# Performance work log

Measured on AMD Instinct MI355X. Metric: run time of the kernel, lower is better.

Reference implementation:

```python
import jax, jax.numpy as jnp
import numpy as np


def setup_inputs() -> dict:
    key = jax.random.key(0)
    ks = jax.random.split(key, 8)
    N, T, U = 8, 512, 64
    E, D, J, V = 512, 512, 512, 500
    s = 0.02
    return {
        "encoder_out": jax.random.normal(ks[0], (N, T, E), jnp.float32),
        "decoder_out": jax.random.normal(ks[1], (N, U, D), jnp.float32),
        "W_enc": jax.random.normal(ks[2], (J, E), jnp.float32) * s,
        "b_enc": jnp.zeros((J,), jnp.float32),
        "W_dec": jax.random.normal(ks[3], (J, D), jnp.float32) * s,
        "b_dec": jnp.zeros((J,), jnp.float32),
        "W_out": jax.random.normal(ks[4], (V, J), jnp.float32) * s,
        "b_out": jnp.zeros((V,), jnp.float32),
    }


def reference(encoder_out, decoder_out, W_enc, b_enc, W_dec, b_dec, W_out, b_out):
    # Project encoder [N,T,E]->[N,T,J] and decoder [N,U,D]->[N,U,J]
    enc = jnp.einsum("nte,je->ntj", encoder_out, W_enc) + b_enc
    dec = jnp.einsum("nud,jd->nuj", decoder_out, W_dec) + b_dec
    # Broadcast add over (T,U), tanh, then vocab projection -> [N,T,U,V]
    activations = jnp.tanh(enc[:, :, None, :] + dec[:, None, :, :])
    logits = jnp.einsum("ntuj,vj->ntuv", activations, W_out) + b_out
    return logits
```

## Files before the change

### kernel.cpp

```cpp
#include <hip/hip_runtime.h>
#include <hip/hip_bf16.h>


typedef __attribute__((ext_vector_type(4))) float f32x4;
typedef __attribute__((ext_vector_type(16))) float f32x16;
typedef __attribute__((ext_vector_type(4))) short s16x4;
typedef __attribute__((ext_vector_type(8))) short s16x8;
typedef __attribute__((ext_vector_type(4))) unsigned short u16x4;

static __device__ __forceinline__ unsigned short f2bf(float x) {
    union { float f; unsigned u; } v; v.f = x;
    return (unsigned short)((v.u + 0x7FFFu + ((v.u >> 16) & 1u)) >> 16);
}

static __device__ __forceinline__ float bf2f(unsigned short u) {
    union { unsigned u; float f; } v; v.u = ((unsigned)u) << 16;
    return v.f;
}

static __device__ __forceinline__ float fast_tanh(float x) {
    float e = __expf(2.0f * x);
    float r = __builtin_amdgcn_rcpf(e + 1.0f);
    return __builtin_fmaf(-2.0f, r, 1.0f);
}

static __device__ __forceinline__ unsigned swz64(int r, int c) {
    return (unsigned)(r * 64 + ((c ^ ((r >> 1) & 3)) << 4));
}

static __device__ void proj_body(
    const float* __restrict__ A, const float* __restrict__ W,
    const float* __restrict__ b, unsigned short* __restrict__ C,
    int mt, int jt, unsigned short* As, unsigned short* Bs)
{
    const int tid = threadIdx.x;
    const int lane = tid & 63, wid = tid >> 6;
    const int wm = wid >> 1, wn = wid & 1;

    f32x4 acc[4][4];
    const f32x4 zero = {0.f, 0.f, 0.f, 0.f};
    #pragma unroll
    for (int i = 0; i < 4; ++i)
        #pragma unroll
        for (int j = 0; j < 4; ++j) acc[i][j] = zero;

    const int c8 = (tid & 7) * 8;
    const int rbase = tid >> 3;

    for (int kt = 0; kt < 8; ++kt) {
        __syncthreads();
        #pragma unroll
        for (int p = 0; p < 4; ++p) {
            int r = p * 32 + rbase;
            int byte = (r * 128 + c8 * 2) ^ ((r & 7) << 4);
            {
                const float* s = A + (size_t)(mt * 128 + r) * 512 + kt * 64 + c8;
                f32x4 v0 = *(const f32x4*)s, v1 = *(const f32x4*)(s + 4);
                s16x8 pk;
                pk[0] = (short)f2bf(v0[0]); pk[1] = (short)f2bf(v0[1]);
                pk[2] = (short)f2bf(v0[2]); pk[3] = (short)f2bf(v0[3]);
                pk[4] = (short)f2bf(v1[0]); pk[5] = (short)f2bf(v1[1]);
                pk[6] = (short)f2bf(v1[2]); pk[7] = (short)f2bf(v1[3]);
                *(s16x8*)((char*)As + byte) = pk;
            }
            {
                const float* s = W + (size_t)(jt * 128 + r) * 512 + kt * 64 + c8;
                f32x4 v0 = *(const f32x4*)s, v1 = *(const f32x4*)(s + 4);
                s16x8 pk;
                pk[0] = (short)f2bf(v0[0]); pk[1] = (short)f2bf(v0[1]);
                pk[2] = (short)f2bf(v0[2]); pk[3] = (short)f2bf(v0[3]);
                pk[4] = (short)f2bf(v1[0]); pk[5] = (short)f2bf(v1[1]);
                pk[6] = (short)f2bf(v1[2]); pk[7] = (short)f2bf(v1[3]);
                *(s16x8*)((char*)Bs + byte) = pk;
            }
        }
        __syncthreads();
        #pragma unroll
        for (int kk = 0; kk < 2; ++kk) {
            s16x8 af[4], bfr[4];
            #pragma unroll
            for (int mi = 0; mi < 4; ++mi) {
                int row = wm * 64 + mi * 16 + (lane & 15);
                int byte = (row * 128 + kk * 64 + ((lane >> 4) * 16)) ^ ((row & 7) << 4);
                af[mi] = *(const s16x8*)((const char*)As + byte);
            }
            #pragma unroll
            for (int ni = 0; ni < 4; ++ni) {
                int row = wn * 64 + ni * 16 + (lane & 15);
                int byte = (row * 128 + kk * 64 + ((lane >> 4) * 16)) ^ ((row & 7) << 4);
                bfr[ni] = *(const s16x8*)((const char*)Bs + byte);
            }
            #pragma unroll
            for (int mi = 0; mi < 4; ++mi)
                #pragma unroll
                for (int ni = 0; ni < 4; ++ni)
                    acc[mi][ni] = __builtin_amdgcn_mfma_f32_16x16x32_bf16(
                        af[mi], bfr[ni], acc[mi][ni], 0, 0, 0);
        }
    }

    #pragma unroll
    for (int ni = 0; ni < 4; ++ni) {
        int col = jt * 128 + wn * 64 + ni * 16 + (lane & 15);
        float bias = b[col];
        #pragma unroll
        for (int mi = 0; mi < 4; ++mi) {
            int row0 = mt * 128 + wm * 64 + mi * 16 + ((lane >> 4) << 2);
            #pragma unroll
            for (int j = 0; j < 4; ++j)
                C[(size_t)(row0 + j) * 512 + col] = f2bf(acc[mi][ni][j] + bias);
        }
    }
}

__global__ __launch_bounds__(256) void prep(
    const float* __restrict__ Wout, unsigned short* __restrict__ img,
    const float* __restrict__ encoder_out, const float* __restrict__ W_enc,
    const float* __restrict__ b_enc, unsigned short* __restrict__ enc_p,
    const float* __restrict__ decoder_out, const float* __restrict__ W_dec,
    const float* __restrict__ b_dec, unsigned short* __restrict__ dec_p,
    const float* __restrict__ b_out, float* __restrict__ bpad)
{
    __shared__ unsigned short As[128 * 64];
    __shared__ unsigned short Bs[128 * 64];
    const int b = blockIdx.x;
    if (b < 128) {
        int tid = b * 256 + threadIdx.x;
        int lane = tid & 63;
        int khalf = (tid >> 6) & 1;
        int tile = (tid >> 7) & 15;
        int kt = tid >> 11;
        int v = tile * 32 + (lane & 31);
        int k = kt * 32 + khalf * 16 + (lane >> 5) * 8;
        s16x8 pk = {0, 0, 0, 0, 0, 0, 0, 0};
        if (v < 500) {
            const float* s = Wout + (size_t)v * 512 + k;
            f32x4 a = *(const f32x4*)s, c = *(const f32x4*)(s + 4);
            pk[0] = (short)f2bf(a[0]); pk[1] = (short)f2bf(a[1]);
            pk[2] = (short)f2bf(a[2]); pk[3] = (short)f2bf(a[3]);
            pk[4] = (short)f2bf(c[0]); pk[5] = (short)f2bf(c[1]);
            pk[6] = (short)f2bf(c[2]); pk[7] = (short)f2bf(c[3]);
        }
        *(s16x8*)(img + (size_t)tid * 8) = pk;
    } else if (b < 256) {
        int q = b - 128;
        proj_body(encoder_out, W_enc, b_enc, enc_p, q & 31, q >> 5, As, Bs);
    } else if (b < 272) {
        int q = b - 256;
        proj_body(decoder_out, W_dec, b_dec, dec_p, q & 3, q >> 2, As, Bs);
    } else {
        int i = threadIdx.x;
        bpad[i] = (i < 500) ? b_out[i] : 0.f;
        bpad[i + 256] = (i + 256 < 500) ? b_out[i + 256] : 0.f;
    }
}

__global__ __launch_bounds__(512, 4) void joiner_main(
    const unsigned short* __restrict__ enc, const unsigned short* __restrict__ dec,
    const unsigned short* __restrict__ Wimg, const float* __restrict__ bout,
    float* __restrict__ out)
{
    __shared__ __align__(16) char raw[66048];
    unsigned short* As0 = (unsigned short*)raw;
    unsigned short* As1 = (unsigned short*)(raw + 4096);
    float* ep = (float*)raw;

    const int bid = blockIdx.x;
    const int tid = threadIdx.x, lane = tid & 63, wn = tid >> 6;
    const int n = bid >> 9, t = bid & 511;

    f32x16 acc[2][2];
    #pragma unroll
    for (int i = 0; i < 2; ++i)
        #pragma unroll
        for (int j = 0; j < 2; ++j)
            #pragma unroll
            for (int e = 0; e < 16; ++e) acc[i][j][e] = 0.f;

    const int r = tid >> 3;
    const int q = tid & 7;
    const unsigned short* erow = enc + ((size_t)n * 512 + t) * 512 + q * 4;
    const unsigned short* drow = dec + ((size_t)n * 64 + r) * 512 + q * 4;
    const unsigned abyte = swz64(r, q >> 1) + (q & 1) * 8;
    const char* wbase = (const char*)Wimg + (size_t)wn * 4096 + (size_t)lane * 16;
    const int lr = lane & 31, kg = lane >> 5;

    {
        u16x4 e = *(const u16x4*)erow;
        u16x4 d = *(const u16x4*)drow;
        s16x4 p;
        p[0] = (short)f2bf(fast_tanh(bf2f(e[0]) + bf2f(d[0])));
        p[1] = (short)f2bf(fast_tanh(bf2f(e[1]) + bf2f(d[1])));
        p[2] = (short)f2bf(fast_tanh(bf2f(e[2]) + bf2f(d[2])));
        p[3] = (short)f2bf(fast_tanh(bf2f(e[3]) + bf2f(d[3])));
        *(s16x4*)((char*)As0 + abyte) = p;
    }
    __syncthreads();

    #pragma unroll
    for (int kt = 0; kt < 16; ++kt) {
        const char* Ac = (char*)((kt & 1) ? As1 : As0);
        char* An = (char*)((kt & 1) ? As0 : As1);
        const char* g = wbase + (size_t)kt * 32768;

        if (kt < 15) {
            u16x4 e = *(const u16x4*)(erow + (kt + 1) * 32);
            u16x4 d = *(const u16x4*)(drow + (kt + 1) * 32);
            s16x4 p;
            p[0] = (short)f2bf(fast_tanh(bf2f(e[0]) + bf2f(d[0])));
            p[1] = (short)f2bf(fast_tanh(bf2f(e[1]) + bf2f(d[1])));
            p[2] = (short)f2bf(fast_tanh(bf2f(e[2]) + bf2f(d[2])));
            p[3] = (short)f2bf(fast_tanh(bf2f(e[3]) + bf2f(d[3])));
            *(s16x4*)(An + abyte) = p;
        }
        #pragma unroll
        for (int kh = 0; kh < 2; ++kh) {
            s16x8 b0 = *(const s16x8*)(g + 0 * 2048 + kh * 1024);
            s16x8 b1 = *(const s16x8*)(g + 1 * 2048 + kh * 1024);
            s16x8 a0 = *(const s16x8*)(Ac + swz64(lr, kh * 2 + kg));
            s16x8 a1 = *(const s16x8*)(Ac + swz64(32 + lr, kh * 2 + kg));
            acc[0][0] = __builtin_amdgcn_mfma_f32_32x32x16_bf16(b0, a0, acc[0][0], 0, 0, 0);
            acc[0][1] = __builtin_amdgcn_mfma_f32_32x32x16_bf16(b1, a0, acc[0][1], 0, 0, 0);
            acc[1][0] = __builtin_amdgcn_mfma_f32_32x32x16_bf16(b0, a1, acc[1][0], 0, 0, 0);
            acc[1][1] = __builtin_amdgcn_mfma_f32_32x32x16_bf16(b1, a1, acc[1][1], 0, 0, 0);
        }
        __syncthreads();
    }

    const int hi4 = (lane >> 5) * 4;
    #pragma unroll
    for (int o = 0; o < 2; ++o) {
        if (o) __syncthreads();
        {
            const int mi = o;
            #pragma unroll
            for (int ni = 0; ni < 2; ++ni) {
                #pragma unroll
                for (int qq = 0; qq < 4; ++qq) {
                    int v4 = wn * 64 + ni * 32 + qq * 8 + hi4;
                    if (v4 < 500) {
                        f32x4 b = *(const f32x4*)(bout + v4);
                        f32x4 ov;
                        ov[0] = acc[mi][ni][qq * 4 + 0] + b[0];
                        ov[1] = acc[mi][ni][qq * 4 + 1] + b[1];
                        ov[2] = acc[mi][ni][qq * 4 + 2] + b[2];
                        ov[3] = acc[mi][ni][qq * 4 + 3] + b[3];
                        *(f32x4*)(ep + lr * 516 + v4) = ov;
                    }
                }
            }
        }
        __syncthreads();
        const size_t obase = ((size_t)bid * 64 + o * 32) * 500;
        #pragma unroll
        for (int i = 0; i < 8; ++i) {
            int idx = i * 512 + tid;
            if (idx < 4000) {
                int rr = idx / 125;
                int vi = (idx - rr * 125) * 4;
                f32x4 ov = *(const f32x4*)(ep + rr * 516 + vi);
                __builtin_nontemporal_store(ov, (f32x4*)(out + obase + (size_t)idx * 4));
            }
        }
    }
}

extern "C" void kernel_launch(void* const* d_in, const int* in_sizes, int n_in,
                              void* d_out, int out_size, void* d_ws, size_t ws_size,
                              hipStream_t stream) {
    const float* encoder_out = (const float*)d_in[0];
    const float* decoder_out = (const float*)d_in[1];
    const float* W_enc = (const float*)d_in[2];
    const float* b_enc = (const float*)d_in[3];
    const float* W_dec = (const float*)d_in[4];
    const float* b_dec = (const float*)d_in[5];
    const float* W_out = (const float*)d_in[6];
    const float* b_out = (const float*)d_in[7];
    float* out = (float*)d_out;

    unsigned short* enc_p = (unsigned short*)d_ws;
    unsigned short* dec_p = enc_p + (size_t)4096 * 512;
    unsigned short* wimg  = dec_p + (size_t)512 * 512;
    float* bpad = (float*)(wimg + 262144);

    prep<<<dim3(273), 256, 0, stream>>>(W_out, wimg,
                                        encoder_out, W_enc, b_enc, enc_p,
                                        decoder_out, W_dec, b_dec, dec_p,
                                        b_out, bpad);
    joiner_main<<<dim3(4096), 512, 0, stream>>>(enc_p, dec_p, wimg, bpad, out);
}
```

Measured before the change: 225.6 us.

## Make joiner persistent over 16 timesteps, overlapping output stores with next MFMA loop

Each block now handles 16 consecutive t positions instead of one, so the grid shrinks from 4096 to 256 blocks. A dedicated epilogue LDS buffer holds the previous timestep's 64x500 tile, and its global stores are spread across the next timestep's k-loop to overlap write traffic with MFMA work. Barriers are replaced by a lighter lgkmcnt wait plus s_barrier, and launch bounds drop to 2 blocks per CU to fit the larger shared memory. The risk is lower parallelism: 256 blocks on a GPU with many CUs may leave CUs idle, and writes per iteration are limited to 500 threads.

```diff
diff --git a/kernel.cpp b/kernel.cpp
--- a/kernel.cpp
+++ b/kernel.cpp
@@ -22,6 +22,12 @@
     float e = __expf(2.0f * x);
     float r = __builtin_amdgcn_rcpf(e + 1.0f);
     return __builtin_fmaf(-2.0f, r, 1.0f);
+}
+
+static __device__ __forceinline__ void lbar() {
+    asm volatile("s_waitcnt lgkmcnt(0)" ::: "memory");
+    __builtin_amdgcn_s_barrier();
+    __builtin_amdgcn_sched_barrier(0);
 }
 
 static __device__ __forceinline__ unsigned swz64(int r, int c) {
@@ -155,38 +161,36 @@
     }
 }
 
-__global__ __launch_bounds__(512, 4) void joiner_main(
+__global__ __launch_bounds__(512, 2) void joiner_main(
     const unsigned short* __restrict__ enc, const unsigned short* __restrict__ dec,
     const unsigned short* __restrict__ Wimg, const float* __restrict__ bout,
     float* __restrict__ out)
 {
-    __shared__ __align__(16) char raw[66048];
+    __shared__ __align__(16) char raw[8192 + 64 * 516 * 4];
     unsigned short* As0 = (unsigned short*)raw;
     unsigned short* As1 = (unsigned short*)(raw + 4096);
-    float* ep = (float*)raw;
+    float* ep = (float*)(raw + 8192);
 
     const int bid = blockIdx.x;
     const int tid = threadIdx.x, lane = tid & 63, wn = tid >> 6;
-    const int n = bid >> 9, t = bid & 511;
-
-    f32x16 acc[2][2];
-    #pragma unroll
-    for (int i = 0; i < 2; ++i)
-        #pragma unroll
-        for (int j = 0; j < 2; ++j)
-            #pragma unroll
-            for (int e = 0; e < 16; ++e) acc[i][j][e] = 0.f;
+    const int n = bid >> 5;
+    const int t0 = (bid & 31) * 16;
 
     const int r = tid >> 3;
     const int q = tid & 7;
-    const unsigned short* erow = enc + ((size_t)n * 512 + t) * 512 + q * 4;
     const unsigned short* drow = dec + ((size_t)n * 64 + r) * 512 + q * 4;
     const unsigned abyte = swz64(r, q >> 1) + (q & 1) * 8;
     const char* wbase = (const char*)Wimg + (size_t)wn * 4096 + (size_t)lane * 16;
     const int lr = lane & 31, kg = lane >> 5;
-
+    const int hi4 = (lane >> 5) * 4;
+
+    const unsigned short* erow0 = enc + ((size_t)n * 512 + t0) * 512 + q * 4;
+
+    f32x16 acc[2][2];
+
+    u16x4 e0, d0;
     {
-        u16x4 e = *(const u16x4*)erow;
+        u16x4 e = *(const u16x4*)erow0;
         u16x4 d = *(const u16x4*)drow;
         s16x4 p;
         p[0] = (short)f2bf(fast_tanh(bf2f(e[0]) + bf2f(d[0])));
@@ -194,45 +198,75 @@
         p[2] = (short)f2bf(fast_tanh(bf2f(e[2]) + bf2f(d[2])));
         p[3] = (short)f2bf(fast_tanh(bf2f(e[3]) + bf2f(d[3])));
         *(s16x4*)((char*)As0 + abyte) = p;
-    }
-    __syncthreads();
-
-    #pragma unroll
-    for (int kt = 0; kt < 16; ++kt) {
-        const char* Ac = (char*)((kt & 1) ? As1 : As0);
-        char* An = (char*)((kt & 1) ? As0 : As1);
-        const char* g = wbase + (size_t)kt * 32768;
-
-        if (kt < 15) {
-            u16x4 e = *(const u16x4*)(erow + (kt + 1) * 32);
-            u16x4 d = *(const u16x4*)(drow + (kt + 1) * 32);
-            s16x4 p;
-            p[0] = (short)f2bf(fast_tanh(bf2f(e[0]) + bf2f(d[0])));
-            p[1] = (short)f2bf(fast_tanh(bf2f(e[1]) + bf2f(d[1])));
-            p[2] = (short)f2bf(fast_tanh(bf2f(e[2]) + bf2f(d[2])));
-            p[3] = (short)f2bf(fast_tanh(bf2f(e[3]) + bf2f(d[3])));
-            *(s16x4*)(An + abyte) = p;
-        }
-        #pragma unroll
-        for (int kh = 0; kh < 2; ++kh) {
-            s16x8 b0 = *(const s16x8*)(g + 0 * 2048 + kh * 1024);
-            s16x8 b1 = *(const s16x8*)(g + 1 * 2048 + kh * 1024);
-            s16x8 a0 = *(const s16x8*)(Ac + swz64(lr, kh * 2 + kg));
-            s16x8 a1 = *(const s16x8*)(Ac + swz64(32 + lr, kh * 2 + kg));
-            acc[0][0] = __builtin_amdgcn_mfma_f32_32x32x16_bf16(b0, a0, acc[0][0], 0, 0, 0);
-            acc[0][1] = __builtin_amdgcn_mfma_f32_32x32x16_bf16(b1, a0, acc[0][1], 0, 0, 0);
-            acc[1][0] = __builtin_amdgcn_mfma_f32_32x32x16_bf16(b0, a1, acc[1][0], 0, 0, 0);
-            acc[1][1] = __builtin_amdgcn_mfma_f32_32x32x16_bf16(b1, a1, acc[1][1], 0, 0, 0);
-        }
-        __syncthreads();
-    }
-
-    const int hi4 = (lane >> 5) * 4;
-    #pragma unroll
-    for (int o = 0; o < 2; ++o) {
-        if (o) __syncthreads();
-        {
-            const int mi = o;
+        e0 = *(const u16x4*)(erow0 + 32);
+        d0 = *(const u16x4*)(drow + 32);
+    }
+    lbar();
+
+    for (int it = 0; it < 16; ++it) {
+        const unsigned short* erow = erow0 + (size_t)it * 512;
+        const size_t pslab = (((size_t)n * 512 + t0 + it - 1) * 64) * 500;
+
+        #pragma unroll
+        for (int i = 0; i < 2; ++i)
+            #pragma unroll
+            for (int j = 0; j < 2; ++j)
+                #pragma unroll
+                for (int el = 0; el < 16; ++el) acc[i][j][el] = 0.f;
+
+        #pragma unroll 2
+        for (int kt = 0; kt < 16; ++kt) {
+            const char* Ac = (char*)((kt & 1) ? As1 : As0);
+            char* An = (char*)((kt & 1) ? As0 : As1);
+
+            const char* g = wbase + (size_t)kt * 32768;
+            s16x8 b00 = *(const s16x8*)(g);
+            s16x8 b0k = *(const s16x8*)(g + 1024);
+            s16x8 b10 = *(const s16x8*)(g + 2048);
+            s16x8 b1k = *(const s16x8*)(g + 3072);
+            if (it > 0 && tid < 500) {
+                int idx = kt * 500 + tid;
+                int rr = idx / 125;
+                int vi = (idx - rr * 125) * 4;
+                f32x4 ov = *(const f32x4*)(ep + rr * 516 + vi);
+                __builtin_nontemporal_store(ov, (f32x4*)(out + pslab + (size_t)idx * 4));
+            }
+            s16x8 a0k0 = *(const s16x8*)(Ac + swz64(lr, kg));
+            s16x8 a1k0 = *(const s16x8*)(Ac + swz64(32 + lr, kg));
+            s16x8 a0k1 = *(const s16x8*)(Ac + swz64(lr, 2 + kg));
+            s16x8 a1k1 = *(const s16x8*)(Ac + swz64(32 + lr, 2 + kg));
+            if (kt < 15) {
+                s16x4 p;
+                p[0] = (short)f2bf(fast_tanh(bf2f(e0[0]) + bf2f(d0[0])));
+                p[1] = (short)f2bf(fast_tanh(bf2f(e0[1]) + bf2f(d0[1])));
+                p[2] = (short)f2bf(fast_tanh(bf2f(e0[2]) + bf2f(d0[2])));
+                p[3] = (short)f2bf(fast_tanh(bf2f(e0[3]) + bf2f(d0[3])));
+                *(s16x4*)(An + abyte) = p;
+                if (kt < 14) {
+                    e0 = *(const u16x4*)(erow + (kt + 2) * 32);
+                    d0 = *(const u16x4*)(drow + (kt + 2) * 32);
+                }
+            }
+            acc[0][0] = __builtin_amdgcn_mfma_f32_32x32x16_bf16(b00, a0k0, acc[0][0], 0, 0, 0);
+            acc[0][1] = __builtin_amdgcn_mfma_f32_32x32x16_bf16(b10, a0k0, acc[0][1], 0, 0, 0);
+            acc[1][0] = __builtin_amdgcn_mfma_f32_32x32x16_bf16(b00, a1k0, acc[1][0], 0, 0, 0);
+            acc[1][1] = __builtin_amdgcn_mfma_f32_32x32x16_bf16(b10, a1k0, acc[1][1], 0, 0, 0);
+            acc[0][0] = __builtin_amdgcn_mfma_f32_32x32x16_bf16(b0k, a0k1, acc[0][0], 0, 0, 0);
+            acc[0][1] = __builtin_amdgcn_mfma_f32_32x32x16_bf16(b1k, a0k1, acc[0][1], 0, 0, 0);
+            acc[1][0] = __builtin_amdgcn_mfma_f32_32x32x16_bf16(b0k, a1k1, acc[1][0], 0, 0, 0);
+            acc[1][1] = __builtin_amdgcn_mfma_f32_32x32x16_bf16(b1k, a1k1, acc[1][1], 0, 0, 0);
+            lbar();
+        }
+
+        u16x4 en, dn;
+        if (it < 15) {
+            en = *(const u16x4*)(erow + 512);
+            dn = *(const u16x4*)drow;
+            e0 = *(const u16x4*)(erow + 512 + 32);
+            d0 = *(const u16x4*)(drow + 32);
+        }
+        #pragma unroll
+        for (int mi = 0; mi < 2; ++mi) {
             #pragma unroll
             for (int ni = 0; ni < 2; ++ni) {
                 #pragma unroll
@@ -245,21 +279,32 @@
                         ov[1] = acc[mi][ni][qq * 4 + 1] + b[1];
                         ov[2] = acc[mi][ni][qq * 4 + 2] + b[2];
                         ov[3] = acc[mi][ni][qq * 4 + 3] + b[3];
-                        *(f32x4*)(ep + lr * 516 + v4) = ov;
+                        *(f32x4*)(ep + (mi * 32 + lr) * 516 + v4) = ov;
                     }
                 }
             }
         }
-        __syncthreads();
-        const size_t obase = ((size_t)bid * 64 + o * 32) * 500;
-        #pragma unroll
-        for (int i = 0; i < 8; ++i) {
-            int idx = i * 512 + tid;
-            if (idx < 4000) {
+        if (it < 15) {
+            s16x4 p;
+            p[0] = (short)f2bf(fast_tanh(bf2f(en[0]) + bf2f(dn[0])));
+            p[1] = (short)f2bf(fast_tanh(bf2f(en[1]) + bf2f(dn[1])));
+            p[2] = (short)f2bf(fast_tanh(bf2f(en[2]) + bf2f(dn[2])));
+            p[3] = (short)f2bf(fast_tanh(bf2f(en[3]) + bf2f(dn[3])));
+            *(s16x4*)((char*)As0 + abyte) = p;
+        }
+        lbar();
+    }
+
+    {
+        const size_t slab = (((size_t)n * 512 + t0 + 15) * 64) * 500;
+        #pragma unroll
+        for (int kt = 0; kt < 16; ++kt) {
+            if (tid < 500) {
+                int idx = kt * 500 + tid;
                 int rr = idx / 125;
                 int vi = (idx - rr * 125) * 4;
                 f32x4 ov = *(const f32x4*)(ep + rr * 516 + vi);
-                __builtin_nontemporal_store(ov, (f32x4*)(out + obase + (size_t)idx * 4));
+                __builtin_nontemporal_store(ov, (f32x4*)(out + slab + (size_t)idx * 4));
             }
         }
     }
@@ -287,5 +332,5 @@
                                         encoder_out, W_enc, b_enc, enc_p,
                                         decoder_out, W_dec, b_dec, dec_p,
                                         b_out, bpad);
-    joiner_main<<<dim3(4096), 512, 0, stream>>>(enc_p, dec_p, wimg, bpad, out);
-}
+    joiner_main<<<dim3(256), 512, 0, stream>>>(enc_p, dec_p, wimg, bpad, out);
+}
```

Result: slower. 255.8 us (+13.4%).
